# Kernel optimization log

Measured on AMD Instinct MI355X. Metric: run time of the kernel, lower is better.

The kernel has to match this reference:

```python
import jax, jax.numpy as jnp
import numpy as np

# thresholds from options['dist_threshold'] (init-time constants)
THRESHOLDS = jnp.array([0.5, 1.0], dtype=jnp.float32)

B, N, D, K = 16, 16384, 64, 64  # batch, h*w pixels, embed dim, n templates
N_CLASSES = 21


def setup_inputs() -> dict:
    key = jax.random.key(0)
    k1, k2, k3 = jax.random.split(key, 3)
    frame_embeddings = jax.random.normal(k1, (B, N, D), dtype=jnp.float32)
    templates = jax.random.normal(k2, (K, N, D), dtype=jnp.float32)
    template_classes = jax.random.randint(k3, (K,), 0, N_CLASSES, dtype=jnp.int64)
    return {
        "frame_embeddings": frame_embeddings,
        "templates": templates,
        "template_classes": template_classes,
    }


def reference(frame_embeddings, templates, template_classes):
    # Squared euclidean distance per pixel to each template, vectorized over K
    # [B,K,N,D] broadcast intermediate the torch loop also never materializes).
    x2 = jnp.sum(frame_embeddings * frame_embeddings, axis=-1)      # [B, N]
    t2 = jnp.sum(templates * templates, axis=-1)                    # [K, N]
    xt = jnp.einsum('bnd,knd->bkn', frame_embeddings, templates)    # [B, K, N]
    dists = x2[:, None, :] + t2[None, :, :] - 2.0 * xt              # [B, K, N]

    min_dists = jnp.min(dists, axis=1)                              # [B, N]
    min_idx = jnp.argmin(dists, axis=1)                             # [B, N]

    # One boolean mask per threshold, stacked: [T, B, N]
    masks = min_dists[None, :, :] <= THRESHOLDS[:, None, None]
    pred_classes = template_classes[min_idx]                        # [B, N]
    return masks, min_dists, pred_classes
```

## Files before the change

kernel.cpp:

```cpp
#include <hip/hip_runtime.h>
#include <stdint.h>


#define BB 16
#define NN 16384
#define DD 64
#define KK 64

__global__ __launch_bounds__(256, 1)
void openset_kernel(const float* __restrict__ x,
                    const float* __restrict__ tmpl,
                    const int*   __restrict__ tcls,
                    float*       __restrict__ out) {
    const int lane = threadIdx.x & 63;
    const int wv   = threadIdx.x >> 6;
    const int n    = blockIdx.x;
    const int d16  = lane & 15;
    const int k4   = lane >> 4;
    const int wb   = wv * 4;

    float4 xv[4];
#pragma unroll
    for (int i = 0; i < 4; ++i)
        xv[i] = *(const float4*)(x + ((size_t)(wb + i) * NN + n) * DD + d16 * 4);

    const float* tb = tmpl + ((size_t)k4 * NN + n) * DD + d16 * 4;

    float bestd = 3.4e38f;
    int   bestk = 0;

    const bool u0 = (lane & 1) != 0;
    const bool u1 = (lane & 2) != 0;

#pragma unroll 8
    for (int cb = 0; cb < KK; cb += 4) {
        float4 tv = *(const float4*)(tb + (size_t)cb * NN * DD);

        float p[4];
#pragma unroll
        for (int i = 0; i < 4; ++i) {
            float d0 = xv[i].x - tv.x;
            float d1 = xv[i].y - tv.y;
            float d2 = xv[i].z - tv.z;
            float d3 = xv[i].w - tv.w;
            p[i] = fmaf(d3, d3, fmaf(d2, d2, fmaf(d1, d1, d0 * d0)));
        }

        float a0 = u0 ? p[2] : p[0];
        float s0 = u0 ? p[0] : p[2];
        float a1 = u0 ? p[3] : p[1];
        float s1 = u0 ? p[1] : p[3];
        float q0 = a0 + __shfl_xor(s0, 1);
        float q1 = a1 + __shfl_xor(s1, 1);
        float a  = u1 ? q1 : q0;
        float s  = u1 ? q0 : q1;
        float r  = a + __shfl_xor(s, 2);
        r += __shfl_xor(r, 4);
        r += __shfl_xor(r, 8);

        const int k = cb + k4;
        if (r < bestd || (r == bestd && k < bestk)) { bestd = r; bestk = k; }
    }

#pragma unroll
    for (int m = 16; m < 64; m <<= 1) {
        float od = __shfl_xor(bestd, m);
        int   ok = __shfl_xor(bestk, m);
        if (od < bestd || (od == bestd && ok < bestk)) { bestd = od; bestk = ok; }
    }

    if (lane < 4) {
        const int b = wb + 2 * (lane & 1) + ((lane >> 1) & 1);
        const size_t BN = (size_t)BB * NN;
        const size_t o  = (size_t)b * NN + n;
        out[o]          = (bestd <= 0.5f) ? 1.0f : 0.0f;
        out[BN + o]     = (bestd <= 1.0f) ? 1.0f : 0.0f;
        out[2 * BN + o] = bestd;
        out[3 * BN + o] = (float)tcls[bestk];
    }
}

extern "C" void kernel_launch(void* const* d_in, const int* in_sizes, int n_in,
                              void* d_out, int out_size, void* d_ws, size_t ws_size,
                              hipStream_t stream) {
    const float* x    = (const float*)d_in[0];
    const float* tmpl = (const float*)d_in[1];
    const int*   tcls = (const int*)d_in[2];
    float* out = (float*)d_out;

    dim3 grid(NN);
    dim3 block(256);
    openset_kernel<<<grid, block, 0, stream>>>(x, tmpl, tcls, out);
}
```

Baseline: 441.6 us.

## Remap lanes to 8 templates per pass with packed float math and swizzles

Lanes now split into 8 d-groups by 8 templates, so each lane loads two float4s per template and covers 8 templates per iteration instead of 4. That halves the loop trip count and shortens the shuffle reduction tree. Arithmetic moves to two-wide vector types so the compiler can emit packed FP32 ops, and the intra-group xor shuffles become ds_swizzle. Block indices are remapped to interleave n across the grid, which changes the DRAM access pattern, and the per-iteration tie-break is simplified because cb increases monotonically.

```diff
diff --git a/kernel.cpp b/kernel.cpp
--- a/kernel.cpp
+++ b/kernel.cpp
@@ -7,6 +7,13 @@
 #define DD 64
 #define KK 64
 
+typedef float v2f __attribute__((ext_vector_type(2)));
+
+template <int PAT>
+__device__ __forceinline__ float swz(float v) {
+    return __int_as_float(__builtin_amdgcn_ds_swizzle(__float_as_int(v), PAT));
+}
+
 __global__ __launch_bounds__(256, 1)
 void openset_kernel(const float* __restrict__ x,
                     const float* __restrict__ tmpl,
@@ -14,56 +21,66 @@
                     float*       __restrict__ out) {
     const int lane = threadIdx.x & 63;
     const int wv   = threadIdx.x >> 6;
-    const int n    = blockIdx.x;
-    const int d16  = lane & 15;
-    const int k4   = lane >> 4;
+    const int n    = ((blockIdx.x & 7) << 11) | (blockIdx.x >> 3);
+    const int d8   = lane & 7;
+    const int k8   = lane >> 3;
     const int wb   = wv * 4;
 
-    float4 xv[4];
+    v2f xlo[4][2], xhi[4][2];
 #pragma unroll
     for (int i = 0; i < 4; ++i)
-        xv[i] = *(const float4*)(x + ((size_t)(wb + i) * NN + n) * DD + d16 * 4);
+#pragma unroll
+        for (int h = 0; h < 2; ++h) {
+            float4 xv = *(const float4*)(x + ((size_t)(wb + i) * NN + n) * DD
+                                           + 4 * d8 + 32 * h);
+            xlo[i][h] = (v2f){xv.x, xv.y};
+            xhi[i][h] = (v2f){xv.z, xv.w};
+        }
 
-    const float* tb = tmpl + ((size_t)k4 * NN + n) * DD + d16 * 4;
+    const float* tb = tmpl + (size_t)k8 * NN * DD + (size_t)n * DD + 4 * d8;
 
-    float bestd = 3.4e38f;
-    int   bestk = 0;
+    float bestd  = 3.4e38f;
+    int   bestcb = 0;
 
     const bool u0 = (lane & 1) != 0;
     const bool u1 = (lane & 2) != 0;
 
-#pragma unroll 8
-    for (int cb = 0; cb < KK; cb += 4) {
-        float4 tv = *(const float4*)(tb + (size_t)cb * NN * DD);
+#pragma unroll
+    for (int cb = 0; cb < KK; cb += 8) {
+        float4 t0 = *(const float4*)(tb + (size_t)cb * NN * DD);
+        float4 t1 = *(const float4*)(tb + (size_t)cb * NN * DD + 32);
+        v2f tl0 = (v2f){t0.x, t0.y}, th0 = (v2f){t0.z, t0.w};
+        v2f tl1 = (v2f){t1.x, t1.y}, th1 = (v2f){t1.z, t1.w};
 
         float p[4];
 #pragma unroll
         for (int i = 0; i < 4; ++i) {
-            float d0 = xv[i].x - tv.x;
-            float d1 = xv[i].y - tv.y;
-            float d2 = xv[i].z - tv.z;
-            float d3 = xv[i].w - tv.w;
-            p[i] = fmaf(d3, d3, fmaf(d2, d2, fmaf(d1, d1, d0 * d0)));
+            v2f dl0 = xlo[i][0] - tl0, dh0 = xhi[i][0] - th0;
+            v2f dl1 = xlo[i][1] - tl1, dh1 = xhi[i][1] - th1;
+            v2f s0v = dl0 * dl0 + dh0 * dh0;
+            v2f s1v = dl1 * dl1 + dh1 * dh1;
+            v2f sv  = s0v + s1v;
+            p[i] = sv.x + sv.y;
         }
 
         float a0 = u0 ? p[2] : p[0];
         float s0 = u0 ? p[0] : p[2];
         float a1 = u0 ? p[3] : p[1];
         float s1 = u0 ? p[1] : p[3];
-        float q0 = a0 + __shfl_xor(s0, 1);
-        float q1 = a1 + __shfl_xor(s1, 1);
+        float q0 = a0 + swz<0x041F>(s0);
+        float q1 = a1 + swz<0x041F>(s1);
         float a  = u1 ? q1 : q0;
         float s  = u1 ? q0 : q1;
-        float r  = a + __shfl_xor(s, 2);
-        r += __shfl_xor(r, 4);
-        r += __shfl_xor(r, 8);
+        float r  = a + swz<0x081F>(s);
+        r += swz<0x101F>(r);
 
-        const int k = cb + k4;
-        if (r < bestd || (r == bestd && k < bestk)) { bestd = r; bestk = k; }
+        if (r < bestd) { bestd = r; bestcb = cb; }
     }
 
+    int bestk = bestcb + k8;
+
 #pragma unroll
-    for (int m = 16; m < 64; m <<= 1) {
+    for (int m = 8; m < 64; m <<= 1) {
         float od = __shfl_xor(bestd, m);
         int   ok = __shfl_xor(bestk, m);
         if (od < bestd || (od == bestd && ok < bestk)) { bestd = od; bestk = ok; }
```

Result: faster. 421.4 us (-4.6%).
